# Optimization experiments

Measured on AMD Instinct MI355X. Metric: run time of the kernel, lower is better.

Reference implementation:

```python
import jax, jax.numpy as jnp
import numpy as np


def _pooled_gray(img):
    # img: [B, C, H, W] -> channel mean then 4x4 average pool -> [B, 1, H/4, W/4]
    m = jnp.mean(img, axis=1, keepdims=True)
    B, _, H, W = m.shape
    return m.reshape(B, 1, H // 4, 4, W // 4, 4).mean(axis=(3, 5))


def _dir_diffs(p):
    # p: [B, 1, h, w]. torch conv2d is cross-correlation with zero padding=1.
    # kernel_left : out[i,j] = p[i,j] - p[i,j-1]
    # kernel_right: out[i,j] = p[i,j] - p[i,j+1]
    # kernel_up   : out[i,j] = p[i,j] - p[i-1,j]
    # kernel_down : out[i,j] = p[i,j] - p[i+1,j]
    pp = jnp.pad(p, ((0, 0), (0, 0), (1, 1), (1, 1)))
    c = pp[:, :, 1:-1, 1:-1]  # == p
    left = c - pp[:, :, 1:-1, :-2]
    right = c - pp[:, :, 1:-1, 2:]
    up = c - pp[:, :, :-2, 1:-1]
    down = c - pp[:, :, 2:, 1:-1]
    return left, right, up, down


def setup_inputs() -> dict:
    key = jax.random.key(0)
    k1, k2 = jax.random.split(key)
    x = jax.random.uniform(k1, (16, 3, 512, 512), dtype=jnp.float32)
    enhance_x = jax.random.uniform(k2, (16, 3, 512, 512), dtype=jnp.float32)
    return {"x": x, "enhance_x": enhance_x}


def reference(x, enhance_x):
    xp = _pooled_gray(x)
    ep = _pooled_gray(enhance_x)
    xl, xr, xu, xd = _dir_diffs(xp)
    el, er, eu, ed = _dir_diffs(ep)
    return (xl - el) ** 2 + (xr - er) ** 2 + (xu - eu) ** 2 + (xd - ed) ** 2
```

## Files before the change

### kernel.cpp

```cpp
#include <hip/hip_runtime.h>


#define B_  16
#define QHW (128 * 128)
#define NQ  (B_ * QHW)

__global__ __launch_bounds__(256) void pool_diff_kernel(
    const float* __restrict__ x, const float* __restrict__ e,
    float* __restrict__ q)
{
    int tid = blockIdx.x * 256 + threadIdx.x;
    int b   = tid >> 14;
    int rem = tid & 16383;
    int i   = rem >> 7;
    int j   = rem & 127;

    const float4* xb = reinterpret_cast<const float4*>(x) + (size_t)b * 3 * 512 * 128;
    const float4* eb = reinterpret_cast<const float4*>(e) + (size_t)b * 3 * 512 * 128;

    int row0 = i << 2;
    float sx = 0.0f, se = 0.0f;
#pragma unroll
    for (int c = 0; c < 3; ++c) {
#pragma unroll
        for (int di = 0; di < 4; ++di) {
            int off = (c * 512 + row0 + di) * 128 + j;
            float4 vx = xb[off];
            float4 ve = eb[off];
            sx += (vx.x + vx.y) + (vx.z + vx.w);
            se += (ve.x + ve.y) + (ve.z + ve.w);
        }
    }
    q[tid] = (sx - se) * (1.0f / 48.0f);
}

__global__ __launch_bounds__(256) void dir_loss_kernel(
    const float* __restrict__ q, float* __restrict__ out)
{
    int tid = blockIdx.x * 256 + threadIdx.x;
    int rem = tid & 16383;
    int i   = rem >> 7;
    int j   = rem & 127;

    const float* qb = q + (tid & ~16383);
    float qc = qb[rem];
    float ql = (j > 0)   ? qb[rem - 1]   : 0.0f;
    float qr = (j < 127) ? qb[rem + 1]   : 0.0f;
    float qu = (i > 0)   ? qb[rem - 128] : 0.0f;
    float qd = (i < 127) ? qb[rem + 128] : 0.0f;

    float dl = qc - ql, dr = qc - qr, du = qc - qu, dd = qc - qd;
    out[tid] = dl * dl + dr * dr + du * du + dd * dd;
}

extern "C" void kernel_launch(void* const* d_in, const int* in_sizes, int n_in,
                              void* d_out, int out_size, void* d_ws, size_t ws_size,
                              hipStream_t stream) {
    const float* x = (const float*)d_in[0];
    const float* e = (const float*)d_in[1];
    float* out = (float*)d_out;
    float* q   = (float*)d_ws;

    dim3 grid(NQ / 256), block(256);
    pool_diff_kernel<<<grid, block, 0, stream>>>(x, e, q);
    dir_loss_kernel<<<grid, block, 0, stream>>>(q, out);
}
```

Before: 114.2 us.

## Fuse pooling and directional loss into one tiled kernel with LDS halo

Merges the pool/diff kernel and the stencil loss kernel into a single launch. Each 512-thread block computes an 18x34 pooled tile, including a one-cell halo, into shared memory and then evaluates the four-direction loss from that tile. This removes the intermediate global buffer round trip and one kernel launch. In exchange, halo cells are recomputed by neighbouring blocks, about 20% extra input reads, and the grid shrinks to 512 blocks, which may lower memory-level parallelism.

```diff
diff --git a/kernel.cpp b/kernel.cpp
--- a/kernel.cpp
+++ b/kernel.cpp
@@ -1,56 +1,54 @@
 #include <hip/hip_runtime.h>
 
 
-#define B_  16
-#define QHW (128 * 128)
-#define NQ  (B_ * QHW)
+__global__ __launch_bounds__(512) void spatial_loss_fused(
+    const float* __restrict__ x, const float* __restrict__ e,
+    float* __restrict__ out)
+{
+    __shared__ float sq[18][35];
 
-__global__ __launch_bounds__(256) void pool_diff_kernel(
-    const float* __restrict__ x, const float* __restrict__ e,
-    float* __restrict__ q)
-{
-    int tid = blockIdx.x * 256 + threadIdx.x;
-    int b   = tid >> 14;
-    int rem = tid & 16383;
-    int i   = rem >> 7;
-    int j   = rem & 127;
+    int blk = blockIdx.x;
+    int b  = blk >> 5;
+    int ti = (blk >> 2) & 7;
+    int tj = blk & 3;
+    int tid = threadIdx.x;
 
     const float4* xb = reinterpret_cast<const float4*>(x) + (size_t)b * 3 * 512 * 128;
     const float4* eb = reinterpret_cast<const float4*>(e) + (size_t)b * 3 * 512 * 128;
 
-    int row0 = i << 2;
-    float sx = 0.0f, se = 0.0f;
+    for (int k = tid; k < 18 * 34; k += 512) {
+        int hy = k / 34, hx = k - hy * 34;
+        int qi = ti * 16 - 1 + hy;
+        int qj = tj * 32 - 1 + hx;
+        float v = 0.0f;
+        if ((unsigned)qi < 128u && (unsigned)qj < 128u) {
+            int row0 = qi << 2;
+            float sx = 0.0f, se = 0.0f;
 #pragma unroll
-    for (int c = 0; c < 3; ++c) {
+            for (int c = 0; c < 3; ++c) {
 #pragma unroll
-        for (int di = 0; di < 4; ++di) {
-            int off = (c * 512 + row0 + di) * 128 + j;
-            float4 vx = xb[off];
-            float4 ve = eb[off];
-            sx += (vx.x + vx.y) + (vx.z + vx.w);
-            se += (ve.x + ve.y) + (ve.z + ve.w);
+                for (int di = 0; di < 4; ++di) {
+                    int off = (c * 512 + row0 + di) * 128 + qj;
+                    float4 vx = xb[off];
+                    float4 ve = eb[off];
+                    sx += (vx.x + vx.y) + (vx.z + vx.w);
+                    se += (ve.x + ve.y) + (ve.z + ve.w);
+                }
+            }
+            v = (sx - se) * (1.0f / 48.0f);
         }
+        sq[hy][hx] = v;
     }
-    q[tid] = (sx - se) * (1.0f / 48.0f);
-}
+    __syncthreads();
 
-__global__ __launch_bounds__(256) void dir_loss_kernel(
-    const float* __restrict__ q, float* __restrict__ out)
-{
-    int tid = blockIdx.x * 256 + threadIdx.x;
-    int rem = tid & 16383;
-    int i   = rem >> 7;
-    int j   = rem & 127;
-
-    const float* qb = q + (tid & ~16383);
-    float qc = qb[rem];
-    float ql = (j > 0)   ? qb[rem - 1]   : 0.0f;
-    float qr = (j < 127) ? qb[rem + 1]   : 0.0f;
-    float qu = (i > 0)   ? qb[rem - 128] : 0.0f;
-    float qd = (i < 127) ? qb[rem + 128] : 0.0f;
-
-    float dl = qc - ql, dr = qc - qr, du = qc - qu, dd = qc - qd;
-    out[tid] = dl * dl + dr * dr + du * du + dd * dd;
+    int ly = tid >> 5, lx = tid & 31;
+    float qc = sq[ly + 1][lx + 1];
+    float dl = qc - sq[ly + 1][lx];
+    float dr = qc - sq[ly + 1][lx + 2];
+    float du = qc - sq[ly][lx + 1];
+    float dd = qc - sq[ly + 2][lx + 1];
+    int qi = ti * 16 + ly, qj = tj * 32 + lx;
+    out[((size_t)b << 14) + (qi << 7) + qj] = dl * dl + dr * dr + du * du + dd * dd;
 }
 
 extern "C" void kernel_launch(void* const* d_in, const int* in_sizes, int n_in,
@@ -59,9 +57,6 @@
     const float* x = (const float*)d_in[0];
     const float* e = (const float*)d_in[1];
     float* out = (float*)d_out;
-    float* q   = (float*)d_ws;
 
-    dim3 grid(NQ / 256), block(256);
-    pool_diff_kernel<<<grid, block, 0, stream>>>(x, e, q);
-    dir_loss_kernel<<<grid, block, 0, stream>>>(q, out);
+    spatial_loss_fused<<<dim3(512), dim3(512), 0, stream>>>(x, e, out);
 }
```

Result: slower. 117.5 us (+2.8%).
